# Performance work log

Measured on AMD Instinct MI355X. Metric: run time of the kernel, lower is better.

The kernel has to match this reference:

```python
import jax, jax.numpy as jnp
import numpy as np

B, S, D = 4, 2048, 256
H = 8
KD = D  # keras MHA key_dim = input_shape[-1] -> per-head dim equals D
EPS = 1e-5


def layer_norm(x, gamma, beta):
    mu = jnp.mean(x, axis=-1, keepdims=True)
    var = jnp.var(x, axis=-1, keepdims=True)
    return (x - mu) * jax.lax.rsqrt(var + EPS) * gamma + beta


def setup_inputs() -> dict:
    key = jax.random.key(0)
    ks = jax.random.split(key, 12)
    scale = 1.0 / np.sqrt(D)
    inp = {
        "input_query": jax.random.normal(ks[0], (B, S, D), jnp.float32),
        "key": jax.random.normal(ks[1], (B, S, D), jnp.float32),
        "value": jax.random.normal(ks[2], (B, S, D), jnp.float32),
        # LayerNorm params (3 separate norms)
        "gq": jnp.ones((D,), jnp.float32), "bq_ln": jnp.zeros((D,), jnp.float32),
        "gk": jnp.ones((D,), jnp.float32), "bk_ln": jnp.zeros((D,), jnp.float32),
        "gv": jnp.ones((D,), jnp.float32), "bv_ln": jnp.zeros((D,), jnp.float32),
        # MHA projection weights: [D, H, KD] for q/k/v, [H, KD, D] for output
        "Wq": jax.random.normal(ks[3], (D, H, KD), jnp.float32) * scale,
        "bq": jnp.zeros((H, KD), jnp.float32),
        "Wk": jax.random.normal(ks[4], (D, H, KD), jnp.float32) * scale,
        "bk": jnp.zeros((H, KD), jnp.float32),
        "Wv": jax.random.normal(ks[5], (D, H, KD), jnp.float32) * scale,
        "bv": jnp.zeros((H, KD), jnp.float32),
        "Wo": jax.random.normal(ks[6], (H, KD, D), jnp.float32) * scale,
        "bo": jnp.zeros((D,), jnp.float32),
    }
    return inp


def reference(input_query, key, value, gq, bq_ln, gk, bk_ln, gv, bv_ln,
              Wq, bq, Wk, bk, Wv, bv, Wo, bo):
    # pre-LN on each stream
    q_in = layer_norm(input_query, gq, bq_ln)
    k_in = layer_norm(key, gk, bk_ln)
    v_in = layer_norm(value, gv, bv_ln)

    # projections -> [B, S, H, KD]
    q = jnp.einsum('bsd,dhk->bshk', q_in, Wq) + bq
    k = jnp.einsum('bsd,dhk->bshk', k_in, Wk) + bk
    v = jnp.einsum('bsd,dhk->bshk', v_in, Wv) + bv

    # scaled dot-product attention (keras scales query by 1/sqrt(key_dim))
    q = q * (1.0 / np.sqrt(KD)).astype(np.float32)
    scores = jnp.einsum('bqhk,bshk->bhqs', q, k)  # [B, H, Sq, Sk]
    probs = jax.nn.softmax(scores, axis=-1)
    # dropout = 0.0 (inference)
    attn = jnp.einsum('bhqs,bshk->bqhk', probs, v)
    out = jnp.einsum('bqhk,hkd->bqd', attn, Wo) + bo

    return input_query + out
```

## Files before the change

### kernel.cpp

```cpp
#include <hip/hip_runtime.h>

using bf16x8 = __attribute__((ext_vector_type(8))) __bf16;
using f32x4  = __attribute__((ext_vector_type(4))) float;
using f32x16 = __attribute__((ext_vector_type(16))) float;
typedef unsigned short u16;
typedef const __attribute__((address_space(1))) void* gas_p;
typedef __attribute__((address_space(3))) void* las_p;

__device__ __forceinline__ u16 f2bf(float f) {
  union { float f; unsigned u; } v; v.f = f;
  unsigned r = v.u + 0x7fffu + ((v.u >> 16) & 1u);
  return (u16)(r >> 16);
}

__device__ __forceinline__ unsigned pkbf(float a, float b) {
  unsigned r;
  asm("v_cvt_pk_bf16_f32 %0, %1, %2" : "=v"(r) : "v"(a), "v"(b));
  return r;
}

__device__ __forceinline__ void gload16(const void* g, void* l) {
  __builtin_amdgcn_global_load_lds((gas_p)g, (las_p)l, 16, 0, 0);
}

#define MFMA(a, b, c)   __builtin_amdgcn_mfma_f32_16x16x32_bf16((a), (b), (c), 0, 0, 0)
#define MFMA32(a, b, c) __builtin_amdgcn_mfma_f32_32x32x16_bf16((a), (b), (c), 0, 0, 0)

__global__ __launch_bounds__(256) void transpose_conv(
    const float* __restrict__ Wq, const float* __restrict__ Wk,
    const float* __restrict__ Wv, const float* __restrict__ Wo,
    u16* __restrict__ wqt, u16* __restrict__ wkt,
    u16* __restrict__ wvt, u16* __restrict__ wot)
{
  int z = blockIdx.y;
  const float* src = (z == 0) ? Wq : (z == 1) ? Wk : (z == 2) ? Wv : Wo;
  u16* dst = (z == 0) ? wqt : (z == 1) ? wkt : (z == 2) ? wvt : wot;
  int C = (z < 3) ? 2048 : 256;
  int R = (z < 3) ? 256 : 2048;
  int TC = C >> 5;
  int tc = blockIdx.x % TC, tr = blockIdx.x / TC;
  __shared__ float tile[32][33];
  int j = threadIdx.x & 31, i0 = threadIdx.x >> 5;
#pragma unroll
  for (int p = 0; p < 4; p++)
    tile[i0 + p * 8][j] = src[(tr * 32 + i0 + p * 8) * C + tc * 32 + j];
  __syncthreads();
#pragma unroll
  for (int p = 0; p < 4; p++)
    dst[(tc * 32 + i0 + p * 8) * R + tr * 32 + j] = f2bf(tile[j][i0 + p * 8]);
}

__global__ __launch_bounds__(256) void ln3_kernel(
    const float* __restrict__ xq, const float* __restrict__ xk, const float* __restrict__ xv,
    const float* __restrict__ gq, const float* __restrict__ bq,
    const float* __restrict__ gk, const float* __restrict__ bk,
    const float* __restrict__ gv, const float* __restrict__ bv,
    u16* __restrict__ oq, u16* __restrict__ ok, u16* __restrict__ ov)
{
  int z = blockIdx.y;
  const float* x = (z == 0) ? xq : (z == 1) ? xk : xv;
  const float* g = (z == 0) ? gq : (z == 1) ? gk : gv;
  const float* be = (z == 0) ? bq : (z == 1) ? bk : bv;
  u16* o = (z == 0) ? oq : (z == 1) ? ok : ov;
  int w = threadIdx.x >> 6, l = threadIdx.x & 63;
  int row = blockIdx.x * 4 + w;
  float4 x4 = *(const float4*)(x + row * 256 + l * 4);
  float s = x4.x + x4.y + x4.z + x4.w;
  float sq = x4.x * x4.x + x4.y * x4.y + x4.z * x4.z + x4.w * x4.w;
#pragma unroll
  for (int mm = 1; mm < 64; mm <<= 1) { s += __shfl_xor(s, mm); sq += __shfl_xor(sq, mm); }
  float mu = s * (1.f / 256.f);
  float var = sq * (1.f / 256.f) - mu * mu;
  float rs = rsqrtf(var + 1e-5f);
  float4 g4 = *(const float4*)(g + l * 4);
  float4 b4 = *(const float4*)(be + l * 4);
  ushort4 o4;
  o4.x = f2bf((x4.x - mu) * rs * g4.x + b4.x);
  o4.y = f2bf((x4.y - mu) * rs * g4.y + b4.y);
  o4.z = f2bf((x4.z - mu) * rs * g4.z + b4.z);
  o4.w = f2bf((x4.w - mu) * rs * g4.w + b4.w);
  *(ushort4*)(o + row * 256 + l * 4) = o4;
}

__global__ __launch_bounds__(256) void proj_gemm(
    const u16* __restrict__ qn, const u16* __restrict__ kn, const u16* __restrict__ vn,
    const u16* __restrict__ wqt, const u16* __restrict__ wkt, const u16* __restrict__ wvt,
    const float* __restrict__ bq, const float* __restrict__ bk, const float* __restrict__ bv,
    u16* __restrict__ qo, u16* __restrict__ ko, u16* __restrict__ vo)
{
  __shared__ u16 As[128 * 64];
  __shared__ u16 Bs[128 * 64];
  int z = blockIdx.z;
  const u16* A  = (z == 0) ? qn : (z == 1) ? kn : vn;
  const u16* Bt = (z == 0) ? wqt : (z == 1) ? wkt : wvt;
  const float* bias = (z == 0) ? bq : (z == 1) ? bk : bv;
  u16* Co = (z == 0) ? qo : (z == 1) ? ko : vo;
  float scale = (z == 0) ? 0.0625f : 1.0f;

  int i0 = blockIdx.x * 128, n0 = blockIdx.y * 128;
  int tid = threadIdx.x, w = tid >> 6, l = tid & 63;
  int wr = w >> 1, wc = w & 1, l15 = l & 15, qv = l >> 4;

  f32x4 acc[4][4] = {};

  for (int k0 = 0; k0 < 256; k0 += 64) {
    __syncthreads();
#pragma unroll
    for (int j = 0; j < 4; j++) {
      int c = (w * 4 + j) * 64 + l;
      int row = c >> 3, co = (c & 7) * 8;
      gload16(A + (i0 + row) * 256 + k0 + co, (char*)As + (w * 4 + j) * 1024);
      gload16(Bt + (n0 + row) * 256 + k0 + co, (char*)Bs + (w * 4 + j) * 1024);
    }
    __syncthreads();
#pragma unroll
    for (int kk = 0; kk < 2; kk++) {
      bf16x8 a[4], bfr[4];
#pragma unroll
      for (int m = 0; m < 4; m++)
        a[m] = *(const bf16x8*)(As + (wr * 64 + m * 16 + l15) * 64 + kk * 32 + qv * 8);
#pragma unroll
      for (int n = 0; n < 4; n++)
        bfr[n] = *(const bf16x8*)(Bs + (wc * 64 + n * 16 + l15) * 64 + kk * 32 + qv * 8);
#pragma unroll
      for (int m = 0; m < 4; m++)
#pragma unroll
        for (int n = 0; n < 4; n++) acc[m][n] = MFMA(a[m], bfr[n], acc[m][n]);
    }
  }

#pragma unroll
  for (int n = 0; n < 4; n++) {
    int col = n0 + wc * 64 + n * 16 + l15;
    float bc = bias[col];
    int h = col >> 8, kd = col & 255;
#pragma unroll
    for (int m = 0; m < 4; m++) {
#pragma unroll
      for (int r = 0; r < 4; r++) {
        int row = i0 + wr * 64 + m * 16 + qv * 4 + r;
        int bb = row >> 11, ss = row & 2047;
        Co[((bb * 8 + h) * 2048 + ss) * 256 + kd] = f2bf((acc[m][n][r] + bc) * scale);
      }
    }
  }
}

__global__ __launch_bounds__(256) void transpose_v_kernel(
    const u16* __restrict__ v, u16* __restrict__ vt)
{
  int bh = blockIdx.y;
  int tc = blockIdx.x & 7, tr = blockIdx.x >> 3;
  const u16* src = v + bh * 2048 * 256;
  u16* dst = vt + bh * 2048 * 256;
  __shared__ u16 tile[32][34];
  int j2 = threadIdx.x & 15, i0 = threadIdx.x >> 4;
#pragma unroll
  for (int p = 0; p < 2; p++) {
    int i = i0 + p * 16;
    unsigned u = *(const unsigned*)(src + (tr * 32 + i) * 256 + tc * 32 + j2 * 2);
    tile[i][j2 * 2] = (u16)u; tile[i][j2 * 2 + 1] = (u16)(u >> 16);
  }
  __syncthreads();
#pragma unroll
  for (int p = 0; p < 2; p++) {
    int i = i0 + p * 16;
    unsigned u = (unsigned)tile[j2 * 2][i] | ((unsigned)tile[j2 * 2 + 1][i] << 16);
    *(unsigned*)(dst + (tc * 32 + i) * 2048 + tr * 32 + j2 * 2) = u;
  }
}

__global__ __launch_bounds__(512, 2) void flash_attn(
    const u16* __restrict__ q, const u16* __restrict__ k,
    const u16* __restrict__ vt, u16* __restrict__ o)
{
  __shared__ char lds[65536];
  int qt = blockIdx.x, bh = blockIdx.y;
  int b = bh >> 3, hh = bh & 7;
  int tid = threadIdx.x, w = tid >> 6, l = tid & 63;
  int l31 = l & 31, h = l >> 5;

  const u16* Q = q + (size_t)(bh * 2048 + qt * 256 + w * 32) * 256;
  const u16* K = k + (size_t)bh * 2048 * 256;
  const u16* V = vt + (size_t)bh * 256 * 2048;

  bf16x8 qf[16];
#pragma unroll
  for (int dt = 0; dt < 16; dt++)
    qf[dt] = *(const bf16x8*)(Q + l31 * 256 + dt * 16 + h * 8);

  f32x16 oacc[8] = {};
  float m_ = -1e30f, lsum = 0.f;

  for (int t = 0; t < 32; t++) {
    __syncthreads();
#pragma unroll
    for (int j = 0; j < 4; j++) {
      int c = w * 4 + j;
      int off = c * 1024 + l * 16;
      {
        int r = off >> 9, ps = l & 31;
        gload16(K + (size_t)(t * 64 + r) * 256 + ((ps ^ (r & 31)) << 3),
                (char*)lds + off);
      }
      {
        int r = off >> 8, ps = l & 15;
        int lsl = ps ^ (r & 15);
        int d = r * 2 + (lsl >> 3);
        gload16(V + (size_t)d * 2048 + t * 64 + ((lsl & 7) << 3),
                (char*)lds + 32768 + off);
      }
    }
    __syncthreads();

    f32x16 p0 = {}, p1 = {};
#pragma unroll
    for (int dt = 0; dt < 16; dt++) {
      int sl = ((dt * 2 + h) ^ l31) << 4;
      bf16x8 kf0 = *(const bf16x8*)((char*)lds + l31 * 512 + sl);
      bf16x8 kf1 = *(const bf16x8*)((char*)lds + (32 + l31) * 512 + sl);
      p0 = MFMA32(kf0, qf[dt], p0);
      p1 = MFMA32(kf1, qf[dt], p1);
    }

    float n0 = fmaxf(fmaxf(p0[0], p0[1]), fmaxf(p0[2], p0[3]));
    float n1 = fmaxf(fmaxf(p0[4], p0[5]), fmaxf(p0[6], p0[7]));
    float n2 = fmaxf(fmaxf(p0[8], p0[9]), fmaxf(p0[10], p0[11]));
    float n3 = fmaxf(fmaxf(p0[12], p0[13]), fmaxf(p0[14], p0[15]));
    float n4 = fmaxf(fmaxf(p1[0], p1[1]), fmaxf(p1[2], p1[3]));
    float n5 = fmaxf(fmaxf(p1[4], p1[5]), fmaxf(p1[6], p1[7]));
    float n6 = fmaxf(fmaxf(p1[8], p1[9]), fmaxf(p1[10], p1[11]));
    float n7 = fmaxf(fmaxf(p1[12], p1[13]), fmaxf(p1[14], p1[15]));
    float mt = fmaxf(fmaxf(fmaxf(n0, n1), fmaxf(n2, n3)),
                     fmaxf(fmaxf(n4, n5), fmaxf(n6, n7)));
    mt = fmaxf(mt, __shfl_xor(mt, 32));
    if (__any(mt > m_ + 8.0f)) {
      float mn = fmaxf(m_, mt);
      float f = __expf(m_ - mn);
      lsum *= f;
#pragma unroll
      for (int dt = 0; dt < 8; dt++)
#pragma unroll
        for (int i = 0; i < 16; i++) oacc[dt][i] *= f;
      m_ = mn;
    }
#pragma unroll
    for (int i = 0; i < 16; i++) { p0[i] = __expf(p0[i] - m_); lsum += p0[i]; }
#pragma unroll
    for (int i = 0; i < 16; i++) { p1[i] = __expf(p1[i] - m_); lsum += p1[i]; }

    unsigned pw[16];
#pragma unroll
    for (int i = 0; i < 8; i++) pw[i] = pkbf(p0[2 * i], p0[2 * i + 1]);
#pragma unroll
    for (int i = 0; i < 8; i++) pw[8 + i] = pkbf(p1[2 * i], p1[2 * i + 1]);

#pragma unroll
    for (int kt = 0; kt < 4; kt++) {
      unsigned x0 = __shfl_xor(pw[4 * kt + 0], 32);
      unsigned x1 = __shfl_xor(pw[4 * kt + 1], 32);
      unsigned x2 = __shfl_xor(pw[4 * kt + 2], 32);
      unsigned x3 = __shfl_xor(pw[4 * kt + 3], 32);
      union { unsigned u[4]; bf16x8 v; } pa;
      pa.u[0] = h ? x2 : pw[4 * kt + 0];
      pa.u[1] = h ? x3 : pw[4 * kt + 1];
      pa.u[2] = h ? pw[4 * kt + 2] : x0;
      pa.u[3] = h ? pw[4 * kt + 3] : x1;
#pragma unroll
      for (int dt = 0; dt < 8; dt++) {
        int d = dt * 32 + l31;
        int r = d >> 1;
        int lsl = (d & 1) * 8 + kt * 2 + h;
        bf16x8 vf = *(const bf16x8*)((char*)lds + 32768 + r * 256 +
                                     ((lsl ^ (r & 15)) << 4));
        oacc[dt] = MFMA32(vf, pa.v, oacc[dt]);
      }
    }
  }

  __syncthreads();
  float inv = 1.0f / (lsum + __shfl_xor(lsum, 32));
  char* wbase = (char*)lds + w * 8192;
  int qr15 = l31 & 15;
#pragma unroll
  for (int ph = 0; ph < 2; ph++) {
    if ((l31 >> 4) == ph) {
#pragma unroll
      for (int dt = 0; dt < 8; dt++) {
#pragma unroll
        for (int rg = 0; rg < 4; rg++) {
          uint2 uu;
          uu.x = pkbf(oacc[dt][rg * 4 + 0] * inv, oacc[dt][rg * 4 + 1] * inv);
          uu.y = pkbf(oacc[dt][rg * 4 + 2] * inv, oacc[dt][rg * 4 + 3] * inv);
          *(uint2*)(wbase + qr15 * 512 + ((dt * 64 + rg * 16) ^ (qr15 << 4)) + h * 8) = uu;
        }
      }
    }
    asm volatile("s_waitcnt lgkmcnt(0)" ::: "memory");
    __builtin_amdgcn_sched_barrier(0);
#pragma unroll
    for (int c = 0; c < 8; c++) {
      int qr = c * 2 + h;
      uint4 vv = *(const uint4*)(wbase + qr * 512 + ((l31 ^ qr) << 4));
      int s = qt * 256 + w * 32 + ph * 16 + qr;
      *(uint4*)((char*)o + (size_t)(b * 2048 + s) * 4096 + hh * 512 + l31 * 16) = vv;
    }
    asm volatile("s_waitcnt lgkmcnt(0)" ::: "memory");
  }
}

__global__ __launch_bounds__(256) void out_gemm(
    const u16* __restrict__ A, const u16* __restrict__ Bt,
    const float* __restrict__ bo, const float* __restrict__ resid,
    float* __restrict__ out)
{
  __shared__ u16 As[128 * 64];
  __shared__ u16 Bs[64 * 64];
  int i0 = blockIdx.x * 128, n0 = blockIdx.y * 64;
  int tid = threadIdx.x, w = tid >> 6, l = tid & 63, l15 = l & 15, qv = l >> 4;

  f32x4 acc[2][4] = {};

  for (int k0 = 0; k0 < 2048; k0 += 64) {
    __syncthreads();
#pragma unroll
    for (int j = 0; j < 4; j++) {
      int c = (w * 4 + j) * 64 + l;
      int row = c >> 3, co = (c & 7) * 8;
      gload16(A + (i0 + row) * 2048 + k0 + co, (char*)As + (w * 4 + j) * 1024);
    }
#pragma unroll
    for (int j = 0; j < 2; j++) {
      int c = (w * 2 + j) * 64 + l;
      int row = c >> 3, co = (c & 7) * 8;
      gload16(Bt + (n0 + row) * 2048 + k0 + co, (char*)Bs + (w * 2 + j) * 1024);
    }
    __syncthreads();
#pragma unroll
    for (int kk = 0; kk < 2; kk++) {
      bf16x8 a[2], bfr[4];
#pragma unroll
      for (int m = 0; m < 2; m++)
        a[m] = *(const bf16x8*)(As + (w * 32 + m * 16 + l15) * 64 + kk * 32 + qv * 8);
#pragma unroll
      for (int n = 0; n < 4; n++)
        bfr[n] = *(const bf16x8*)(Bs + (n * 16 + l15) * 64 + kk * 32 + qv * 8);
#pragma unroll
      for (int m = 0; m < 2; m++)
#pragma unroll
        for (int n = 0; n < 4; n++) acc[m][n] = MFMA(a[m], bfr[n], acc[m][n]);
    }
  }

#pragma unroll
  for (int n = 0; n < 4; n++) {
    int col = n0 + n * 16 + l15;
    float bc = bo[col];
#pragma unroll
    for (int m = 0; m < 2; m++)
#pragma unroll
      for (int r = 0; r < 4; r++) {
        int row = i0 + w * 32 + m * 16 + qv * 4 + r;
        out[row * 256 + col] = acc[m][n][r] + bc + resid[row * 256 + col];
      }
  }
}

extern "C" void kernel_launch(void* const* d_in, const int* in_sizes, int n_in,
                              void* d_out, int out_size, void* d_ws, size_t ws_size,
                              hipStream_t stream)
{
  const float* inq  = (const float*)d_in[0];
  const float* key  = (const float*)d_in[1];
  const float* val  = (const float*)d_in[2];
  const float* gq   = (const float*)d_in[3];
  const float* bqln = (const float*)d_in[4];
  const float* gk   = (const float*)d_in[5];
  const float* bkln = (const float*)d_in[6];
  const float* gv   = (const float*)d_in[7];
  const float* bvln = (const float*)d_in[8];
  const float* Wq   = (const float*)d_in[9];
  const float* bq   = (const float*)d_in[10];
  const float* Wk   = (const float*)d_in[11];
  const float* bk   = (const float*)d_in[12];
  const float* Wv   = (const float*)d_in[13];
  const float* bv   = (const float*)d_in[14];
  const float* Wo   = (const float*)d_in[15];
  const float* bo   = (const float*)d_in[16];

  char* ws = (char*)d_ws;
  const size_t MB = 1ull << 20;
  u16* wqt = (u16*)(ws + 0 * MB);
  u16* wkt = (u16*)(ws + 1 * MB);
  u16* wvt = (u16*)(ws + 2 * MB);
  u16* wot = (u16*)(ws + 3 * MB);
  u16* qn  = (u16*)(ws + 4 * MB);
  u16* kn  = (u16*)(ws + 8 * MB);
  u16* vn  = (u16*)(ws + 12 * MB);
  u16* qws = (u16*)(ws + 16 * MB);
  u16* kws = (u16*)(ws + 48 * MB);
  u16* vws = (u16*)(ws + 80 * MB);
  u16* vtw = (u16*)(ws + 112 * MB);
  u16* attn = vws;

  transpose_conv<<<dim3(512, 4), 256, 0, stream>>>(Wq, Wk, Wv, Wo, wqt, wkt, wvt, wot);
  ln3_kernel<<<dim3(2048, 3), 256, 0, stream>>>(inq, key, val, gq, bqln, gk, bkln, gv, bvln,
                                                qn, kn, vn);
  proj_gemm<<<dim3(64, 16, 3), 256, 0, stream>>>(qn, kn, vn, wqt, wkt, wvt, bq, bk, bv,
                                                 qws, kws, vws);
  transpose_v_kernel<<<dim3(512, 32), 256, 0, stream>>>(vws, vtw);
  flash_attn<<<dim3(8, 32), 512, 0, stream>>>(qws, kws, vtw, attn);
  out_gemm<<<dim3(64, 4), 256, 0, stream>>>(attn, wot, bo, inq, (float*)d_out);
}
```

Measured before the change: 298.6 us.

## Fuse V transpose into projection epilogue and double-buffer flash attention K/V tiles

The V projection epilogue now writes V directly in transposed [b,h,kd,s] layout with 4-wide vector stores, which removes the separate transpose kernel and its extra round trip through global memory. Flash attention double-buffers K/V tiles in 128KB of LDS, prefetching the next tile while computing the current one, and raises wave priority around the MFMA loops. The grid is flattened to 1D with a remapped block-to-(qt,bh) order, presumably for cache locality. The doubled LDS footprint likely drops occupancy from two blocks per CU to one.

```diff
diff --git a/kernel.cpp b/kernel.cpp
--- a/kernel.cpp
+++ b/kernel.cpp
@@ -129,44 +129,40 @@
     }
   }
 
-#pragma unroll
-  for (int n = 0; n < 4; n++) {
-    int col = n0 + wc * 64 + n * 16 + l15;
-    float bc = bias[col];
-    int h = col >> 8, kd = col & 255;
-#pragma unroll
-    for (int m = 0; m < 4; m++) {
-#pragma unroll
-      for (int r = 0; r < 4; r++) {
-        int row = i0 + wr * 64 + m * 16 + qv * 4 + r;
-        int bb = row >> 11, ss = row & 2047;
-        Co[((bb * 8 + h) * 2048 + ss) * 256 + kd] = f2bf((acc[m][n][r] + bc) * scale);
-      }
-    }
-  }
-}
-
-__global__ __launch_bounds__(256) void transpose_v_kernel(
-    const u16* __restrict__ v, u16* __restrict__ vt)
-{
-  int bh = blockIdx.y;
-  int tc = blockIdx.x & 7, tr = blockIdx.x >> 3;
-  const u16* src = v + bh * 2048 * 256;
-  u16* dst = vt + bh * 2048 * 256;
-  __shared__ u16 tile[32][34];
-  int j2 = threadIdx.x & 15, i0 = threadIdx.x >> 4;
-#pragma unroll
-  for (int p = 0; p < 2; p++) {
-    int i = i0 + p * 16;
-    unsigned u = *(const unsigned*)(src + (tr * 32 + i) * 256 + tc * 32 + j2 * 2);
-    tile[i][j2 * 2] = (u16)u; tile[i][j2 * 2 + 1] = (u16)(u >> 16);
-  }
-  __syncthreads();
-#pragma unroll
-  for (int p = 0; p < 2; p++) {
-    int i = i0 + p * 16;
-    unsigned u = (unsigned)tile[j2 * 2][i] | ((unsigned)tile[j2 * 2 + 1][i] << 16);
-    *(unsigned*)(dst + (tc * 32 + i) * 2048 + tr * 32 + j2 * 2) = u;
+  if (z == 2) {
+#pragma unroll
+    for (int n = 0; n < 4; n++) {
+      int col = n0 + wc * 64 + n * 16 + l15;
+      float bc = bias[col];
+      int h = col >> 8, kd = col & 255;
+#pragma unroll
+      for (int m = 0; m < 4; m++) {
+        int row0 = i0 + wr * 64 + m * 16 + qv * 4;
+        int bb = row0 >> 11, ss = row0 & 2047;
+        ushort4 o4;
+        o4.x = f2bf(acc[m][n][0] + bc);
+        o4.y = f2bf(acc[m][n][1] + bc);
+        o4.z = f2bf(acc[m][n][2] + bc);
+        o4.w = f2bf(acc[m][n][3] + bc);
+        *(ushort4*)(Co + ((size_t)(bb * 8 + h) * 256 + kd) * 2048 + ss) = o4;
+      }
+    }
+  } else {
+#pragma unroll
+    for (int n = 0; n < 4; n++) {
+      int col = n0 + wc * 64 + n * 16 + l15;
+      float bc = bias[col];
+      int h = col >> 8, kd = col & 255;
+#pragma unroll
+      for (int m = 0; m < 4; m++) {
+#pragma unroll
+        for (int r = 0; r < 4; r++) {
+          int row = i0 + wr * 64 + m * 16 + qv * 4 + r;
+          int bb = row >> 11, ss = row & 2047;
+          Co[((bb * 8 + h) * 2048 + ss) * 256 + kd] = f2bf((acc[m][n][r] + bc) * scale);
+        }
+      }
+    }
   }
 }
 
@@ -174,8 +170,10 @@
     const u16* __restrict__ q, const u16* __restrict__ k,
     const u16* __restrict__ vt, u16* __restrict__ o)
 {
-  __shared__ char lds[65536];
-  int qt = blockIdx.x, bh = blockIdx.y;
+  __shared__ char lds[131072];
+  int f = blockIdx.x;
+  int qt = f >> 5;
+  int bh = (f & 7) | (((f >> 3) & 3) << 3);
   int b = bh >> 3, hh = bh & 7;
   int tid = threadIdx.x, w = tid >> 6, l = tid & 63;
   int l31 = l & 31, h = l >> 5;
@@ -192,36 +190,43 @@
   f32x16 oacc[8] = {};
   float m_ = -1e30f, lsum = 0.f;
 
-  for (int t = 0; t < 32; t++) {
-    __syncthreads();
+  auto stage = [&](int t, char* base) {
 #pragma unroll
     for (int j = 0; j < 4; j++) {
       int c = w * 4 + j;
       int off = c * 1024 + l * 16;
       {
         int r = off >> 9, ps = l & 31;
-        gload16(K + (size_t)(t * 64 + r) * 256 + ((ps ^ (r & 31)) << 3),
-                (char*)lds + off);
+        gload16(K + (size_t)(t * 64 + r) * 256 + ((ps ^ (r & 31)) << 3), base + off);
       }
       {
         int r = off >> 8, ps = l & 15;
         int lsl = ps ^ (r & 15);
         int d = r * 2 + (lsl >> 3);
-        gload16(V + (size_t)d * 2048 + t * 64 + ((lsl & 7) << 3),
-                (char*)lds + 32768 + off);
-      }
-    }
-    __syncthreads();
+        gload16(V + (size_t)d * 2048 + t * 64 + ((lsl & 7) << 3), base + 32768 + off);
+      }
+    }
+  };
+
+  stage(0, lds);
+  __syncthreads();
+
+  for (int t = 0; t < 32; t++) {
+    char* cur = lds + (size_t)(t & 1) * 65536;
+    char* nxt = lds + (size_t)((t + 1) & 1) * 65536;
+    if (t + 1 < 32) stage(t + 1, nxt);
 
     f32x16 p0 = {}, p1 = {};
+    __builtin_amdgcn_s_setprio(1);
 #pragma unroll
     for (int dt = 0; dt < 16; dt++) {
       int sl = ((dt * 2 + h) ^ l31) << 4;
-      bf16x8 kf0 = *(const bf16x8*)((char*)lds + l31 * 512 + sl);
-      bf16x8 kf1 = *(const bf16x8*)((char*)lds + (32 + l31) * 512 + sl);
+      bf16x8 kf0 = *(const bf16x8*)(cur + l31 * 512 + sl);
+      bf16x8 kf1 = *(const bf16x8*)(cur + (32 + l31) * 512 + sl);
       p0 = MFMA32(kf0, qf[dt], p0);
       p1 = MFMA32(kf1, qf[dt], p1);
     }
+    __builtin_amdgcn_s_setprio(0);
 
     float n0 = fmaxf(fmaxf(p0[0], p0[1]), fmaxf(p0[2], p0[3]));
     float n1 = fmaxf(fmaxf(p0[4], p0[5]), fmaxf(p0[6], p0[7]));
@@ -236,12 +241,12 @@
     mt = fmaxf(mt, __shfl_xor(mt, 32));
     if (__any(mt > m_ + 8.0f)) {
       float mn = fmaxf(m_, mt);
-      float f = __expf(m_ - mn);
-      lsum *= f;
+      float fsc = __expf(m_ - mn);
+      lsum *= fsc;
 #pragma unroll
       for (int dt = 0; dt < 8; dt++)
 #pragma unroll
-        for (int i = 0; i < 16; i++) oacc[dt][i] *= f;
+        for (int i = 0; i < 16; i++) oacc[dt][i] *= fsc;
       m_ = mn;
     }
 #pragma unroll
@@ -266,16 +271,20 @@
       pa.u[1] = h ? x3 : pw[4 * kt + 1];
       pa.u[2] = h ? pw[4 * kt + 2] : x0;
       pa.u[3] = h ? pw[4 * kt + 3] : x1;
+      __builtin_amdgcn_s_setprio(1);
 #pragma unroll
       for (int dt = 0; dt < 8; dt++) {
         int d = dt * 32 + l31;
         int r = d >> 1;
         int lsl = (d & 1) * 8 + kt * 2 + h;
-        bf16x8 vf = *(const bf16x8*)((char*)lds + 32768 + r * 256 +
-                                     ((lsl ^ (r & 15)) << 4));
+        bf16x8 vf = *(const bf16x8*)(cur + 32768 + r * 256 + ((lsl ^ (r & 15)) << 4));
         oacc[dt] = MFMA32(vf, pa.v, oacc[dt]);
       }
-    }
+      __builtin_amdgcn_s_setprio(0);
+    }
+
+    asm volatile("s_waitcnt vmcnt(0)" ::: "memory");
+    __syncthreads();
   }
 
   __syncthreads();
@@ -399,16 +408,14 @@
   u16* vn  = (u16*)(ws + 12 * MB);
   u16* qws = (u16*)(ws + 16 * MB);
   u16* kws = (u16*)(ws + 48 * MB);
-  u16* vws = (u16*)(ws + 80 * MB);
+  u16* attn = (u16*)(ws + 80 * MB);
   u16* vtw = (u16*)(ws + 112 * MB);
-  u16* attn = vws;
 
   transpose_conv<<<dim3(512, 4), 256, 0, stream>>>(Wq, Wk, Wv, Wo, wqt, wkt, wvt, wot);
   ln3_kernel<<<dim3(2048, 3), 256, 0, stream>>>(inq, key, val, gq, bqln, gk, bkln, gv, bvln,
                                                 qn, kn, vn);
   proj_gemm<<<dim3(64, 16, 3), 256, 0, stream>>>(qn, kn, vn, wqt, wkt, wvt, bq, bk, bv,
-                                                 qws, kws, vws);
-  transpose_v_kernel<<<dim3(512, 32), 256, 0, stream>>>(vws, vtw);
-  flash_attn<<<dim3(8, 32), 512, 0, stream>>>(qws, kws, vtw, attn);
+                                                 qws, kws, vtw);
+  flash_attn<<<256, 512, 0, stream>>>(qws, kws, vtw, attn);
   out_gemm<<<dim3(64, 4), 256, 0, stream>>>(attn, wot, bo, inq, (float*)d_out);
 }
```

Result: faster. 267.3 us (-10.5%).
